# Kernel tuning notes

Hardware: AMD Instinct MI355X
Metric: run time of the kernel (lower is better)

## Reference

```python
import jax, jax.numpy as jnp
import numpy as np

NH = 12   # num_heads
EPS = 1e-6


def _layer_norm(x):
    m = jnp.mean(x, axis=-1, keepdims=True)
    v = jnp.mean((x - m) ** 2, axis=-1, keepdims=True)
    return (x - m) * jax.lax.rsqrt(v + EPS)


def _rms_norm(x, w):
    return x * jax.lax.rsqrt(jnp.mean(x * x, axis=-1, keepdims=True) + EPS) * w


def _rope_cos_sin(f, h, w, head_dim):
    # matches rope_params + calculate_freqs_i: split c=head_dim//2 complex freqs
    # into [c-2*(c//3), c//3, c//3] for the (F,H,W) axes.
    c = head_dim // 2
    inv = 1.0 / (10000.0 ** (np.arange(0, head_dim, 2, dtype=np.float64) / head_dim))
    c1 = c - 2 * (c // 3); c2 = c // 3
    af = np.outer(np.arange(f), inv[:c1])
    ah = np.outer(np.arange(h), inv[c1:c1 + c2])
    aw = np.outer(np.arange(w), inv[c1 + c2:])
    ang = np.concatenate([
        np.broadcast_to(af[:, None, None, :], (f, h, w, c1)),
        np.broadcast_to(ah[None, :, None, :], (f, h, w, c2)),
        np.broadcast_to(aw[None, None, :, :], (f, h, w, c2)),
    ], axis=-1).reshape(f * h * w, c)
    return jnp.asarray(np.cos(ang), jnp.float32), jnp.asarray(np.sin(ang), jnp.float32)


def _apply_rope(x, cos, sin):
    # complex rotation on interleaved pairs; x: [B,L,n,d]
    B, L, n, d = x.shape
    xr = x.reshape(B, L, n, d // 2, 2)
    x0, x1 = xr[..., 0], xr[..., 1]
    co = cos[None, :, None, :]; si = sin[None, :, None, :]
    return jnp.stack([x0 * co - x1 * si, x0 * si + x1 * co], axis=-1).reshape(B, L, n, d)


def _attention(q, k, v):
    scale = 1.0 / jnp.sqrt(jnp.asarray(q.shape[-1], q.dtype))
    s = jnp.einsum('blnd,bmnd->bnlm', q, k) * scale
    return jnp.einsum('bnlm,bmnd->blnd', jax.nn.softmax(s, axis=-1), v)


def _block(x, e, context, mod, sa_wq, sa_bq, sa_wk, sa_bk, sa_wv, sa_bv, sa_wo, sa_bo,
           sa_nq, sa_nk, n3_w, n3_b, ca_wq, ca_bq, ca_wk, ca_bk, ca_wv, ca_bv, ca_wo,
           ca_bo, ca_nq, ca_nk, ffn_w1, ffn_b1, ffn_w2, ffn_b2, f, h, w):
    B, L, C = x.shape
    D = C // NH
    em = mod + e                      # [B,6,C] AdaLN shift/scale/gate params
    cos, sin = _rope_cos_sin(f, h, w, D)
    # --- self-attention with AdaLN modulation + RoPE + qk RMSNorm ---
    xa = _layer_norm(x) * (1.0 + em[:, 1:2]) + em[:, 0:1]
    q = _rms_norm(xa @ sa_wq + sa_bq, sa_nq).reshape(B, L, NH, D)
    k = _rms_norm(xa @ sa_wk + sa_bk, sa_nk).reshape(B, L, NH, D)
    v = (xa @ sa_wv + sa_bv).reshape(B, L, NH, D)
    q = _apply_rope(q, cos, sin)
    k = _apply_rope(k, cos, sin)
    y = _attention(q, k, v).reshape(B, L, C) @ sa_wo + sa_bo
    x = x + y * em[:, 2:3]
    # --- t2v cross-attention (norm3 is affine LayerNorm) ---
    L2 = context.shape[1]
    xc = _layer_norm(x) * n3_w + n3_b
    q = _rms_norm(xc @ ca_wq + ca_bq, ca_nq).reshape(B, L, NH, D)
    k = _rms_norm(context @ ca_wk + ca_bk, ca_nk).reshape(B, L2, NH, D)
    v = (context @ ca_wv + ca_bv).reshape(B, L2, NH, D)
    x = x + (_attention(q, k, v).reshape(B, L, C) @ ca_wo + ca_bo)
    # --- FFN (GELU-tanh) with AdaLN modulation ---
    xf = _layer_norm(x) * (1.0 + em[:, 4:5]) + em[:, 3:4]
    y = jax.nn.gelu(xf @ ffn_w1 + ffn_b1, approximate=True) @ ffn_w2 + ffn_b2
    return x + y * em[:, 5:6]


def setup_inputs() -> dict:
    key = jax.random.key(0)
    ks = jax.random.split(key, 16)
    B, L2, C, FFN = 1, 512, 1536, 8960
    F, H, W = 9, 16, 28
    L = F * H * W  # 4032
    def mk(i, shape, s=0.02):
        return jax.random.normal(ks[i], shape, jnp.float32) * s
    return {
        'x': jax.random.normal(ks[0], (B, L, C), jnp.float32),
        'e': jax.random.normal(ks[1], (B, 6, C), jnp.float32),
        'context': jax.random.normal(ks[2], (B, L2, C), jnp.float32),
        'mod': jax.random.normal(ks[3], (1, 6, C), jnp.float32) / jnp.sqrt(float(C)),
        'sa_wq': mk(4, (C, C)), 'sa_bq': jnp.zeros((C,), jnp.float32),
        'sa_wk': mk(5, (C, C)), 'sa_bk': jnp.zeros((C,), jnp.float32),
        'sa_wv': mk(6, (C, C)), 'sa_bv': jnp.zeros((C,), jnp.float32),
        'sa_wo': mk(7, (C, C)), 'sa_bo': jnp.zeros((C,), jnp.float32),
        'sa_nq': jnp.ones((C,), jnp.float32), 'sa_nk': jnp.ones((C,), jnp.float32),
        'n3_w': jnp.ones((C,), jnp.float32), 'n3_b': jnp.zeros((C,), jnp.float32),
        'ca_wq': mk(8, (C, C)), 'ca_bq': jnp.zeros((C,), jnp.float32),
        'ca_wk': mk(9, (C, C)), 'ca_bk': jnp.zeros((C,), jnp.float32),
        'ca_wv': mk(10, (C, C)), 'ca_bv': jnp.zeros((C,), jnp.float32),
        'ca_wo': mk(11, (C, C)), 'ca_bo': jnp.zeros((C,), jnp.float32),
        'ca_nq': jnp.ones((C,), jnp.float32), 'ca_nk': jnp.ones((C,), jnp.float32),
        'ffn_w1': mk(12, (C, FFN)), 'ffn_b1': jnp.zeros((FFN,), jnp.float32),
        'ffn_w2': mk(13, (FFN, C)), 'ffn_b2': jnp.zeros((C,), jnp.float32),
        'f': F, 'h': H, 'w': W,
    }


def reference(x, e, context, mod, sa_wq, sa_bq, sa_wk, sa_bk, sa_wv, sa_bv, sa_wo,
              sa_bo, sa_nq, sa_nk, n3_w, n3_b, ca_wq, ca_bq, ca_wk, ca_bk, ca_wv,
              ca_bv, ca_wo, ca_bo, ca_nq, ca_nk, ffn_w1, ffn_b1, ffn_w2, ffn_b2,
              f, h, w):
    return _block(x, e, context, mod, sa_wq, sa_bq, sa_wk, sa_bk, sa_wv, sa_bv,
                  sa_wo, sa_bo, sa_nq, sa_nk, n3_w, n3_b, ca_wq, ca_bq, ca_wk,
                  ca_bk, ca_wv, ca_bv, ca_wo, ca_bo, ca_nq, ca_nk, ffn_w1, ffn_b1,
                  ffn_w2, ffn_b2, f, h, w)
```

## Files before the change

### kernel.cpp

```cpp
#include <hip/hip_runtime.h>
#include <math.h>


#define L_SEQ 4032
#define L_PAD 4096
#define C_DIM 1536
#define L_CTX 512
#define FFN_DIM 8960
#define NHEAD 12
#define DHEAD 128

typedef __attribute__((ext_vector_type(8))) short short8;
typedef __attribute__((ext_vector_type(4))) float floatx4;

__device__ inline unsigned short f2bf(float x) {
  unsigned int u = __float_as_uint(x);
  u += 0x7fffu + ((u >> 16) & 1u);
  return (unsigned short)(u >> 16);
}

__device__ inline float2 block_sum2(float2 v) {
  __shared__ float2 red[4];
#pragma unroll
  for (int o = 32; o > 0; o >>= 1) {
    v.x += __shfl_xor(v.x, o, 64);
    v.y += __shfl_xor(v.y, o, 64);
  }
  int wave = threadIdx.x >> 6;
  if ((threadIdx.x & 63) == 0) red[wave] = v;
  __syncthreads();
  float2 t = make_float2(0.f, 0.f);
#pragma unroll
  for (int i = 0; i < 4; ++i) { t.x += red[i].x; t.y += red[i].y; }
  return t;
}

__global__ void add_kernel(float* __restrict__ o, const float* __restrict__ a,
                           const float* __restrict__ b, int n) {
  int i = blockIdx.x * 256 + threadIdx.x;
  if (i < n) o[i] = a[i] + b[i];
}

__global__ void concat3_kernel(float* __restrict__ o, const float* __restrict__ a,
                               const float* __restrict__ b, const float* __restrict__ c) {
  int i = blockIdx.x * 256 + threadIdx.x;
  if (i < C_DIM) {
    o[i] = a[i];
    o[C_DIM + i] = b[i];
    if (c) o[2 * C_DIM + i] = c[i];
  }
}

__global__ void f32_to_bf16_kernel(unsigned short* __restrict__ o,
                                   const float* __restrict__ in, int n) {
  int i = (blockIdx.x * 256 + threadIdx.x) * 4;
  if (i < n) {
    float4 v = *(const float4*)&in[i];
    ushort4 o4 = {f2bf(v.x), f2bf(v.y), f2bf(v.z), f2bf(v.w)};
    *(ushort4*)&o[i] = o4;
  }
}

__global__ __launch_bounds__(256) void transpose_bf16_kernel(
    const float* __restrict__ W, unsigned short* __restrict__ WT, int K, int N) {
  __shared__ float t[32][33];
  int n0 = blockIdx.x * 32, k0 = blockIdx.y * 32;
  int c = threadIdx.x & 31, r0 = threadIdx.x >> 5;
#pragma unroll
  for (int i = 0; i < 4; ++i) {
    int r = r0 + 8 * i;
    t[r][c] = W[(size_t)(k0 + r) * N + n0 + c];
  }
  __syncthreads();
#pragma unroll
  for (int i = 0; i < 4; ++i) {
    int r = r0 + 8 * i;
    WT[(size_t)(n0 + r) * K + k0 + c] = f2bf(t[c][r]);
  }
}

__global__ __launch_bounds__(256) void transpose_v_kernel(
    const float* __restrict__ V, unsigned short* __restrict__ Vt, int stride, int Lk) {
  __shared__ float t[32][33];
  int k0 = blockIdx.x * 32, c0 = blockIdx.y * 32;
  int c = threadIdx.x & 31, r0 = threadIdx.x >> 5;
#pragma unroll
  for (int i = 0; i < 4; ++i) {
    int r = r0 + 8 * i;
    t[r][c] = V[(size_t)(k0 + r) * stride + c0 + c];
  }
  __syncthreads();
#pragma unroll
  for (int i = 0; i < 4; ++i) {
    int r = r0 + 8 * i;
    Vt[(size_t)(c0 + r) * Lk + k0 + c] = f2bf(t[c][r]);
  }
}

__global__ __launch_bounds__(256) void ln_affine_kernel(
    unsigned short* __restrict__ out, const float* __restrict__ in,
    const float* __restrict__ sc, const float* __restrict__ sh, float addOne) {
  int row = blockIdx.x;
  const float* xr = in + (size_t)row * C_DIM;
  float vals[C_DIM / 256];
  float2 p = make_float2(0.f, 0.f);
  int cnt = 0;
  for (int c = threadIdx.x; c < C_DIM; c += 256) {
    float v = xr[c];
    vals[cnt++] = v;
    p.x += v; p.y += v * v;
  }
  float2 t = block_sum2(p);
  float mean = t.x * (1.f / C_DIM);
  float var = t.y * (1.f / C_DIM) - mean * mean;
  float r = rsqrtf(var + 1e-6f);
  cnt = 0;
  for (int c = threadIdx.x; c < C_DIM; c += 256) {
    float xh = (vals[cnt++] - mean) * r;
    out[(size_t)row * C_DIM + c] = f2bf(xh * (addOne + sc[c]) + sh[c]);
  }
}

template <int ROPE>
__global__ __launch_bounds__(256) void rms_post_kernel(
    unsigned short* __restrict__ obf, const float* __restrict__ in,
    const float* __restrict__ w, const float* __restrict__ cosb,
    const float* __restrict__ sinb, int stride, float ps) {
  int row = blockIdx.x;
  const float* xr = in + (size_t)row * stride;
  int c0 = threadIdx.x * 6;
  float v[6];
  *(float2*)&v[0] = *(const float2*)&xr[c0];
  *(float2*)&v[2] = *(const float2*)&xr[c0 + 2];
  *(float2*)&v[4] = *(const float2*)&xr[c0 + 4];
  float s2 = 0.f;
#pragma unroll
  for (int i = 0; i < 6; ++i) s2 += v[i] * v[i];
  float2 t = block_sum2(make_float2(s2, 0.f));
  float r = rsqrtf(t.x * (1.f / C_DIM) + 1e-6f) * ps;
#pragma unroll
  for (int i = 0; i < 6; ++i) v[i] *= r * w[c0 + i];
  if (ROPE) {
#pragma unroll
    for (int i = 0; i < 3; ++i) {
      int c = c0 + 2 * i;
      int j = (c & 127) >> 1;
      float co = cosb[row * 64 + j], si = sinb[row * 64 + j];
      float a = v[2 * i], b = v[2 * i + 1];
      v[2 * i] = a * co - b * si;
      v[2 * i + 1] = a * si + b * co;
    }
  }
  unsigned short* op = obf + (size_t)row * C_DIM + c0;
  ushort2 o01 = {f2bf(v[0]), f2bf(v[1])};
  ushort2 o23 = {f2bf(v[2]), f2bf(v[3])};
  ushort2 o45 = {f2bf(v[4]), f2bf(v[5])};
  *(ushort2*)&op[0] = o01;
  *(ushort2*)&op[2] = o23;
  *(ushort2*)&op[4] = o45;
}

__global__ void rope_tables_kernel(float* __restrict__ cosb, float* __restrict__ sinb) {
  int l = blockIdx.x, j = threadIdx.x;
  int f = l / (16 * 28);
  int rem = l % (16 * 28);
  int hh = rem / 28, ww = rem % 28;
  double inv = pow(10000.0, -(double)(2 * j) / 128.0);
  double pos = (j < 22) ? (double)f : ((j < 43) ? (double)hh : (double)ww);
  double ang = pos * inv;
  cosb[l * 64 + j] = (float)cos(ang);
  sinb[l * 64 + j] = (float)sin(ang);
}

__device__ inline float gelu_tanh(float x) {
  float x3 = x * x * x;
  return 0.5f * x * (1.f + tanhf(0.79788456080286535588f * (x + 0.044715f * x3)));
}

__device__ inline int xcd_remap(int flat, int nwg) {
  int qq = nwg >> 3, rr = nwg & 7;
  int xcd = flat & 7, idx = flat >> 3;
  return (xcd < rr ? xcd * (qq + 1) : rr * (qq + 1) + (xcd - rr) * qq) + idx;
}

template <int EPI>
__global__ __launch_bounds__(256) void mgemm_kernel(
    const unsigned short* __restrict__ A, const unsigned short* __restrict__ BT,
    const float* __restrict__ bias, void* __restrict__ Cout,
    const float* __restrict__ resid, const float* __restrict__ gate,
    int N, int K, int Mlimit) {
  __shared__ short sA[3][4096];
  __shared__ short sB[3][4096];
  const int tid = threadIdx.x;
  const int wv = tid >> 6, lane = tid & 63;
  const int lm = lane & 15, lq = lane >> 4;
  const int wr = wv >> 1, wc = wv & 1;

  const int gx = gridDim.x;
  int flat = xcd_remap(blockIdx.y * gx + blockIdx.x, gx * gridDim.y);
  const int row0 = (flat / gx) * 128, col0 = (flat % gx) * 128;

  floatx4 zero4 = {0.f, 0.f, 0.f, 0.f};
  floatx4 acc[4][4];
#pragma unroll
  for (int i = 0; i < 4; ++i)
#pragma unroll
    for (int j = 0; j < 4; ++j) acc[i][j] = zero4;

  const unsigned short* Abase = A + ((size_t)row0 + lm) * K + lq * 8;
  const unsigned short* Bbase = BT + ((size_t)col0 + lm) * K + lq * 8;

  auto stage = [&](int buf, int k0) {
#pragma unroll
    for (int t = 0; t < 2; ++t) {
      int g = wv * 2 + t;
      __builtin_amdgcn_global_load_lds(
          (const __attribute__((address_space(1))) void*)(Abase + (size_t)(g * 16) * K + k0),
          (__attribute__((address_space(3))) void*)(sA[buf] + g * 512), 16, 0, 0);
      __builtin_amdgcn_global_load_lds(
          (const __attribute__((address_space(1))) void*)(Bbase + (size_t)(g * 16) * K + k0),
          (__attribute__((address_space(3))) void*)(sB[buf] + g * 512), 16, 0, 0);
    }
  };

  stage(0, 0);
  stage(1, 32);
  asm volatile("s_waitcnt vmcnt(4)" ::: "memory");
  __builtin_amdgcn_s_barrier();
  __builtin_amdgcn_sched_barrier(0);

  int cur = 0;
  const int nk = K >> 5;
  for (int t = 0; t < nk; ++t) {
    int b2 = cur + 2; if (b2 >= 3) b2 -= 3;
    const bool more = (t + 2 < nk);
    if (more) stage(b2, (t + 2) << 5);
    const short* sAc = &sA[cur][0];
    const short* sBc = &sB[cur][0];
    short8 af[4], bfv[4];
#pragma unroll
    for (int mt = 0; mt < 4; ++mt)
      af[mt] = *(const short8*)(sAc + (wr * 4 + mt) * 512 + lane * 8);
#pragma unroll
    for (int nt = 0; nt < 4; ++nt)
      bfv[nt] = *(const short8*)(sBc + (wc * 4 + nt) * 512 + lane * 8);
#pragma unroll
    for (int mt = 0; mt < 4; ++mt)
#pragma unroll
      for (int nt = 0; nt < 4; ++nt)
        acc[mt][nt] = __builtin_amdgcn_mfma_f32_16x16x32_bf16(
            af[mt], bfv[nt], acc[mt][nt], 0, 0, 0);
    __builtin_amdgcn_sched_barrier(0);
    if (more) { asm volatile("s_waitcnt vmcnt(4)" ::: "memory"); }
    else      { asm volatile("s_waitcnt vmcnt(0)" ::: "memory"); }
    __builtin_amdgcn_s_barrier();
    __builtin_amdgcn_sched_barrier(0);
    cur = (cur + 1 == 3) ? 0 : cur + 1;
  }

#pragma unroll
  for (int nt = 0; nt < 4; ++nt) {
    int colg = col0 + wc * 64 + nt * 16 + lm;
    float bv = bias[colg];
    float gv = (EPI == 2 && gate) ? gate[colg] : 1.f;
#pragma unroll
    for (int mt = 0; mt < 4; ++mt) {
#pragma unroll
      for (int r = 0; r < 4; ++r) {
        int rowg = row0 + wr * 64 + mt * 16 + lq * 4 + r;
        if (rowg < Mlimit) {
          float v = acc[mt][nt][r] + bv;
          if (EPI == 1) {
            ((unsigned short*)Cout)[(size_t)rowg * N + colg] = f2bf(gelu_tanh(v));
          } else if (EPI == 2) {
            ((float*)Cout)[(size_t)rowg * N + colg] =
                resid[(size_t)rowg * N + colg] + v * gv;
          } else {
            ((float*)Cout)[(size_t)rowg * N + colg] = v;
          }
        }
      }
    }
  }
}

template <int EPI>
__global__ __launch_bounds__(256) void mgemm_k64_kernel(
    const unsigned short* __restrict__ A, const unsigned short* __restrict__ BT,
    const float* __restrict__ bias, void* __restrict__ Cout,
    const float* __restrict__ resid, const float* __restrict__ gate,
    int N, int K, int Mlimit) {
  __shared__ short sA[2][8192];
  __shared__ short sB[2][8192];
  const int tid = threadIdx.x;
  const int wv = tid >> 6, lane = tid & 63;
  const int lm = lane & 15, lq = lane >> 4;
  const int wr = wv >> 1, wc = wv & 1;

  const int gx = gridDim.x;
  int flat = xcd_remap(blockIdx.y * gx + blockIdx.x, gx * gridDim.y);
  const int row0 = (flat / gx) * 128, col0 = (flat % gx) * 128;

  floatx4 zero4 = {0.f, 0.f, 0.f, 0.f};
  floatx4 acc[4][4];
#pragma unroll
  for (int i = 0; i < 4; ++i)
#pragma unroll
    for (int j = 0; j < 4; ++j) acc[i][j] = zero4;

  const unsigned short* Abase = A + ((size_t)row0 + lm) * K + lq * 8;
  const unsigned short* Bbase = BT + ((size_t)col0 + lm) * K + lq * 8;

  auto stage = [&](int buf, int k0) {
#pragma unroll
    for (int kk = 0; kk < 2; ++kk) {
#pragma unroll
      for (int t = 0; t < 2; ++t) {
        int g = wv * 2 + t;
        __builtin_amdgcn_global_load_lds(
            (const __attribute__((address_space(1))) void*)(Abase + (size_t)(g * 16) * K + k0 + kk * 32),
            (__attribute__((address_space(3))) void*)(sA[buf] + kk * 4096 + g * 512), 16, 0, 0);
        __builtin_amdgcn_global_load_lds(
            (const __attribute__((address_space(1))) void*)(Bbase + (size_t)(g * 16) * K + k0 + kk * 32),
            (__attribute__((address_space(3))) void*)(sB[buf] + kk * 4096 + g * 512), 16, 0, 0);
      }
    }
  };

  stage(0, 0);
  asm volatile("s_waitcnt vmcnt(0)" ::: "memory");
  __builtin_amdgcn_s_barrier();
  __builtin_amdgcn_sched_barrier(0);

  int cur = 0;
  const int nk = K >> 6;
  for (int t = 0; t < nk; ++t) {
    if (t + 1 < nk) stage(cur ^ 1, (t + 1) << 6);
#pragma unroll
    for (int kk = 0; kk < 2; ++kk) {
      const short* sAc = &sA[cur][kk * 4096];
      const short* sBc = &sB[cur][kk * 4096];
      short8 af[4], bfv[4];
#pragma unroll
      for (int mt = 0; mt < 4; ++mt)
        af[mt] = *(const short8*)(sAc + (wr * 4 + mt) * 512 + lane * 8);
#pragma unroll
      for (int nt = 0; nt < 4; ++nt)
        bfv[nt] = *(const short8*)(sBc + (wc * 4 + nt) * 512 + lane * 8);
#pragma unroll
      for (int mt = 0; mt < 4; ++mt)
#pragma unroll
        for (int nt = 0; nt < 4; ++nt)
          acc[mt][nt] = __builtin_amdgcn_mfma_f32_16x16x32_bf16(
              af[mt], bfv[nt], acc[mt][nt], 0, 0, 0);
    }
    __builtin_amdgcn_sched_barrier(0);
    asm volatile("s_waitcnt vmcnt(0)" ::: "memory");
    __builtin_amdgcn_s_barrier();
    __builtin_amdgcn_sched_barrier(0);
    cur ^= 1;
  }

#pragma unroll
  for (int nt = 0; nt < 4; ++nt) {
    int colg = col0 + wc * 64 + nt * 16 + lm;
    float bv = bias[colg];
    float gv = (EPI == 2 && gate) ? gate[colg] : 1.f;
#pragma unroll
    for (int mt = 0; mt < 4; ++mt) {
#pragma unroll
      for (int r = 0; r < 4; ++r) {
        int rowg = row0 + wr * 64 + mt * 16 + lq * 4 + r;
        if (rowg < Mlimit) {
          float v = acc[mt][nt][r] + bv;
          if (EPI == 1) {
            ((unsigned short*)Cout)[(size_t)rowg * N + colg] = f2bf(gelu_tanh(v));
          } else if (EPI == 2) {
            ((float*)Cout)[(size_t)rowg * N + colg] =
                resid[(size_t)rowg * N + colg] + v * gv;
          } else {
            ((float*)Cout)[(size_t)rowg * N + colg] = v;
          }
        }
      }
    }
  }
}

template <int EPI>
__global__ __launch_bounds__(256) void mgemm64_kernel(
    const unsigned short* __restrict__ A, const unsigned short* __restrict__ BT,
    const float* __restrict__ bias, void* __restrict__ Cout,
    const float* __restrict__ resid, const float* __restrict__ gate,
    int N, int K, int Mlimit) {
  __shared__ short sA[3][2048];
  __shared__ short sB[3][4096];
  const int tid = threadIdx.x;
  const int wv = tid >> 6, lane = tid & 63;
  const int lm = lane & 15, lq = lane >> 4;
  const int wc = wv;

  const int gx = gridDim.x;
  int flat = xcd_remap(blockIdx.y * gx + blockIdx.x, gx * gridDim.y);
  const int row0 = (flat / gx) * 64, col0 = (flat % gx) * 128;

  floatx4 zero4 = {0.f, 0.f, 0.f, 0.f};
  floatx4 acc[4][2];
#pragma unroll
  for (int i = 0; i < 4; ++i)
#pragma unroll
    for (int j = 0; j < 2; ++j) acc[i][j] = zero4;

  const unsigned short* Abase = A + ((size_t)row0 + lm) * K + lq * 8;
  const unsigned short* Bbase = BT + ((size_t)col0 + lm) * K + lq * 8;

  auto stage = [&](int buf, int k0) {
    __builtin_amdgcn_global_load_lds(
        (const __attribute__((address_space(1))) void*)(Abase + (size_t)(wv * 16) * K + k0),
        (__attribute__((address_space(3))) void*)(sA[buf] + wv * 512), 16, 0, 0);
#pragma unroll
    for (int t = 0; t < 2; ++t) {
      int g = wv * 2 + t;
      __builtin_amdgcn_global_load_lds(
          (const __attribute__((address_space(1))) void*)(Bbase + (size_t)(g * 16) * K + k0),
          (__attribute__((address_space(3))) void*)(sB[buf] + g * 512), 16, 0, 0);
    }
  };

  stage(0, 0);
  stage(1, 32);
  asm volatile("s_waitcnt vmcnt(3)" ::: "memory");
  __builtin_amdgcn_s_barrier();
  __builtin_amdgcn_sched_barrier(0);

  int cur = 0;
  const int nk = K >> 5;
  for (int t = 0; t < nk; ++t) {
    int b2 = cur + 2; if (b2 >= 3) b2 -= 3;
    const bool more = (t + 2 < nk);
    if (more) stage(b2, (t + 2) << 5);
    const short* sAc = &sA[cur][0];
    const short* sBc = &sB[cur][0];
    short8 af[4], bfv[2];
#pragma unroll
    for (int mt = 0; mt < 4; ++mt)
      af[mt] = *(const short8*)(sAc + mt * 512 + lane * 8);
#pragma unroll
    for (int nt = 0; nt < 2; ++nt)
      bfv[nt] = *(const short8*)(sBc + (wc * 2 + nt) * 512 + lane * 8);
#pragma unroll
    for (int mt = 0; mt < 4; ++mt)
#pragma unroll
      for (int nt = 0; nt < 2; ++nt)
        acc[mt][nt] = __builtin_amdgcn_mfma_f32_16x16x32_bf16(
            af[mt], bfv[nt], acc[mt][nt], 0, 0, 0);
    __builtin_amdgcn_sched_barrier(0);
    if (more) { asm volatile("s_waitcnt vmcnt(3)" ::: "memory"); }
    else      { asm volatile("s_waitcnt vmcnt(0)" ::: "memory"); }
    __builtin_amdgcn_s_barrier();
    __builtin_amdgcn_sched_barrier(0);
    cur = (cur + 1 == 3) ? 0 : cur + 1;
  }

#pragma unroll
  for (int nt = 0; nt < 2; ++nt) {
    int colg = col0 + wc * 32 + nt * 16 + lm;
    float bv = bias[colg];
    float gv = (EPI == 2 && gate) ? gate[colg] : 1.f;
#pragma unroll
    for (int mt = 0; mt < 4; ++mt) {
#pragma unroll
      for (int r = 0; r < 4; ++r) {
        int rowg = row0 + mt * 16 + lq * 4 + r;
        if (rowg < Mlimit) {
          float v = acc[mt][nt][r] + bv;
          if (EPI == 1) {
            ((unsigned short*)Cout)[(size_t)rowg * N + colg] = f2bf(gelu_tanh(v));
          } else if (EPI == 2) {
            ((float*)Cout)[(size_t)rowg * N + colg] =
                resid[(size_t)rowg * N + colg] + v * gv;
          } else {
            ((float*)Cout)[(size_t)rowg * N + colg] = v;
          }
        }
      }
    }
  }
}

__global__ __launch_bounds__(256) void attn_mfma_kernel(
    const unsigned short* __restrict__ Qb, const unsigned short* __restrict__ Kb,
    const unsigned short* __restrict__ Vt, unsigned short* __restrict__ O,
    int Lk) {
  __shared__ short sK[3][4096];
  __shared__ short sV[3][4096];
  __shared__ short sP[4][512];
  const int h = blockIdx.y;
  const int q0 = blockIdx.x * 64;
  const int tid = threadIdx.x;
  const int wv = tid >> 6, lane = tid & 63;
  const int lm = lane & 15, lq = lane >> 4;

  short8 qf[4];
  {
    const unsigned short* qrow =
        Qb + (size_t)(q0 + wv * 16 + lm) * C_DIM + h * DHEAD + lq * 8;
#pragma unroll
    for (int dc = 0; dc < 4; ++dc) qf[dc] = *(const short8*)(qrow + dc * 32);
  }

  floatx4 zero4 = {0.f, 0.f, 0.f, 0.f};
  floatx4 acc[8];
#pragma unroll
  for (int g = 0; g < 8; ++g) acc[g] = zero4;
  float m = -1e30f, l = 0.f;

  auto stageKV = [&](int buf, int k0) {
#pragma unroll
    for (int t = 0; t < 2; ++t) {
      int g = wv * 2 + t;
      int nt_ = g >> 2, dc = g & 3;
      const unsigned short* srck =
          Kb + (size_t)(k0 + nt_ * 16 + lm) * C_DIM + h * DHEAD + dc * 32 + lq * 8;
      __builtin_amdgcn_global_load_lds(
          (const __attribute__((address_space(1))) void*)srck,
          (__attribute__((address_space(3))) void*)(sK[buf] + g * 512), 16, 0, 0);
      const unsigned short* srcv =
          Vt + (size_t)(h * DHEAD + g * 16 + lm) * Lk + k0 + lq * 8;
      __builtin_amdgcn_global_load_lds(
          (const __attribute__((address_space(1))) void*)srcv,
          (__attribute__((address_space(3))) void*)(sV[buf] + g * 512), 16, 0, 0);
    }
  };

  stageKV(0, 0);
  stageKV(1, 32);
  asm volatile("s_waitcnt vmcnt(4)" ::: "memory");
  __builtin_amdgcn_s_barrier();
  __builtin_amdgcn_sched_barrier(0);

  int cur = 0;
  const int nsteps = Lk >> 5;
  for (int t = 0; t < nsteps; ++t) {
    int b2 = cur + 2; if (b2 >= 3) b2 -= 3;
    const bool more = (t + 2 < nsteps);
    if (more) stageKV(b2, (t + 2) << 5);
    const short* sKc = &sK[cur][0];
    const short* sVc = &sV[cur][0];

    floatx4 s0 = zero4, s1 = zero4;
#pragma unroll
    for (int dc = 0; dc < 4; ++dc) {
      short8 kf0 = *(const short8*)(sKc + dc * 512 + lane * 8);
      short8 kf1 = *(const short8*)(sKc + (4 + dc) * 512 + lane * 8);
      s0 = __builtin_amdgcn_mfma_f32_16x16x32_bf16(kf0, qf[dc], s0, 0, 0, 0);
      s1 = __builtin_amdgcn_mfma_f32_16x16x32_bf16(kf1, qf[dc], s1, 0, 0, 0);
    }

    float mx = fmaxf(fmaxf(fmaxf(s0[0], s0[1]), fmaxf(s0[2], s0[3])),
                     fmaxf(fmaxf(s1[0], s1[1]), fmaxf(s1[2], s1[3])));
    mx = fmaxf(mx, __shfl_xor(mx, 16));
    mx = fmaxf(mx, __shfl_xor(mx, 32));
    bool need = mx > m + 11.5f;
    if (__any((int)need)) {
      float mn = fmaxf(m, mx);
      float al = exp2f(m - mn);
      m = mn;
      l *= al;
      float ar[4];
#pragma unroll
      for (int r = 0; r < 4; ++r) ar[r] = __shfl(al, lq * 4 + r);
#pragma unroll
      for (int g = 0; g < 8; ++g)
#pragma unroll
        for (int r = 0; r < 4; ++r) acc[g][r] *= ar[r];
    }
    float rs = 0.f;
    ushort4 pk0, pk1;
#pragma unroll
    for (int r = 0; r < 4; ++r) {
      float p = exp2f(s0[r] - m);
      rs += p;
      ((unsigned short*)&pk0)[r] = f2bf(p);
    }
#pragma unroll
    for (int r = 0; r < 4; ++r) {
      float p = exp2f(s1[r] - m);
      rs += p;
      ((unsigned short*)&pk1)[r] = f2bf(p);
    }
    rs += __shfl_xor(rs, 16);
    rs += __shfl_xor(rs, 32);
    l += rs;
    {
      int baseq = (((lq >> 1) * 16 + lm) << 3) + ((lq & 1) << 2);
      *(ushort4*)&sP[wv][baseq] = pk0;
      *(ushort4*)&sP[wv][baseq + 256] = pk1;
    }
    asm volatile("" ::: "memory");
    short8 pa = *(const short8*)(&sP[wv][lane * 8]);
#pragma unroll
    for (int g = 0; g < 8; ++g) {
      short8 vf = *(const short8*)(sVc + g * 512 + lane * 8);
      acc[g] = __builtin_amdgcn_mfma_f32_16x16x32_bf16(pa, vf, acc[g], 0, 0, 0);
    }
    __builtin_amdgcn_sched_barrier(0);
    if (more) { asm volatile("s_waitcnt vmcnt(4)" ::: "memory"); }
    else      { asm volatile("s_waitcnt vmcnt(0)" ::: "memory"); }
    __builtin_amdgcn_s_barrier();
    __builtin_amdgcn_sched_barrier(0);
    cur = (cur + 1 == 3) ? 0 : cur + 1;
  }

  float invl[4];
#pragma unroll
  for (int r = 0; r < 4; ++r) invl[r] = 1.f / __shfl(l, lq * 4 + r);
  unsigned short* orow =
      O + (size_t)(q0 + wv * 16 + lq * 4) * C_DIM + h * DHEAD + lm;
#pragma unroll
  for (int g = 0; g < 8; ++g) {
#pragma unroll
    for (int r = 0; r < 4; ++r) {
      orow[(size_t)r * C_DIM + g * 16] = f2bf(acc[g][r] * invl[r]);
    }
  }
}

extern "C" void kernel_launch(void* const* d_in, const int* in_sizes, int n_in,
                              void* d_out, int out_size, void* d_ws, size_t ws_size,
                              hipStream_t stream) {
  const float* x     = (const float*)d_in[0];
  const float* e     = (const float*)d_in[1];
  const float* ctx   = (const float*)d_in[2];
  const float* mod   = (const float*)d_in[3];
  const float* sa_wq = (const float*)d_in[4];
  const float* sa_bq = (const float*)d_in[5];
  const float* sa_wk = (const float*)d_in[6];
  const float* sa_bk = (const float*)d_in[7];
  const float* sa_wv = (const float*)d_in[8];
  const float* sa_bv = (const float*)d_in[9];
  const float* sa_wo = (const float*)d_in[10];
  const float* sa_bo = (const float*)d_in[11];
  const float* sa_nq = (const float*)d_in[12];
  const float* sa_nk = (const float*)d_in[13];
  const float* n3_w  = (const float*)d_in[14];
  const float* n3_b  = (const float*)d_in[15];
  const float* ca_wq = (const float*)d_in[16];
  const float* ca_bq = (const float*)d_in[17];
  const float* ca_wk = (const float*)d_in[18];
  const float* ca_bk = (const float*)d_in[19];
  const float* ca_wv = (const float*)d_in[20];
  const float* ca_bv = (const float*)d_in[21];
  const float* ca_wo = (const float*)d_in[22];
  const float* ca_bo = (const float*)d_in[23];
  const float* ca_nq = (const float*)d_in[24];
  const float* ca_nk = (const float*)d_in[25];
  const float* ffn_w1 = (const float*)d_in[26];
  const float* ffn_b1 = (const float*)d_in[27];
  const float* ffn_w2 = (const float*)d_in[28];
  const float* ffn_b2 = (const float*)d_in[29];
  float* out = (float*)d_out;

  char* wsb = (char*)d_ws;
  auto alloc_f = [&](size_t n) { float* p = (float*)wsb; wsb += ((n * 4 + 255) / 256) * 256; return p; };
  auto alloc_h = [&](size_t n) { unsigned short* p = (unsigned short*)wsb; wsb += ((n * 2 + 255) / 256) * 256; return p; };

  float* em   = alloc_f(6 * C_DIM);
  float* cosb = alloc_f(L_SEQ * 64);
  float* sinb = alloc_f(L_SEQ * 64);
  float* qkv  = alloc_f((size_t)L_SEQ * 3 * C_DIM);
  float* x1b  = alloc_f((size_t)L_SEQ * C_DIM);
  unsigned short* act_bf  = alloc_h((size_t)L_PAD * C_DIM);
  unsigned short* ctx_bf  = alloc_h((size_t)L_CTX * C_DIM);
  unsigned short* wtqkv = alloc_h((size_t)3 * C_DIM * C_DIM);
  unsigned short* wto   = alloc_h((size_t)C_DIM * C_DIM);
  unsigned short* wtcq  = alloc_h((size_t)C_DIM * C_DIM);
  unsigned short* wtckv = alloc_h((size_t)2 * C_DIM * C_DIM);
  unsigned short* wtco  = alloc_h((size_t)C_DIM * C_DIM);
  unsigned short* wt1   = alloc_h((size_t)FFN_DIM * C_DIM);
  unsigned short* wt2   = alloc_h((size_t)C_DIM * FFN_DIM);
  float* qkv_bias = alloc_f(3 * C_DIM);
  float* ckv_bias = alloc_f(2 * C_DIM);
  unsigned short* kbf_x = alloc_h((size_t)L_CTX * C_DIM);
  unsigned short* vtx   = alloc_h((size_t)C_DIM * L_CTX);

  unsigned short* qbf_self = (unsigned short*)x1b;
  unsigned short* kbf_self = ((unsigned short*)x1b) + (size_t)L_SEQ * C_DIM;
  unsigned short* vt_self  = (unsigned short*)out;
  unsigned short* qbf_x    = (unsigned short*)out;
  float* crossq = qkv;
  float* ckv    = qkv + (size_t)L_SEQ * C_DIM;
  unsigned short* ffnh_bf = (unsigned short*)qkv;

  const float qscale = 0.12751649737103347f;

  dim3 gT(C_DIM / 32, C_DIM / 32);
  dim3 gQKV(3 * C_DIM / 128, L_PAD / 128);
  dim3 gGL64(C_DIM / 128, L_PAD / 64);
  dim3 gCKV64(2 * C_DIM / 128, L_CTX / 64);
  dim3 gAtt(L_SEQ / 64, NHEAD);

  transpose_bf16_kernel<<<gT, 256, 0, stream>>>(sa_wq, wtqkv, C_DIM, C_DIM);
  transpose_bf16_kernel<<<gT, 256, 0, stream>>>(sa_wk, wtqkv + (size_t)C_DIM * C_DIM, C_DIM, C_DIM);
  transpose_bf16_kernel<<<gT, 256, 0, stream>>>(sa_wv, wtqkv + (size_t)2 * C_DIM * C_DIM, C_DIM, C_DIM);
  transpose_bf16_kernel<<<gT, 256, 0, stream>>>(sa_wo, wto, C_DIM, C_DIM);
  transpose_bf16_kernel<<<gT, 256, 0, stream>>>(ca_wq, wtcq, C_DIM, C_DIM);
  transpose_bf16_kernel<<<gT, 256, 0, stream>>>(ca_wk, wtckv, C_DIM, C_DIM);
  transpose_bf16_kernel<<<gT, 256, 0, stream>>>(ca_wv, wtckv + (size_t)C_DIM * C_DIM, C_DIM, C_DIM);
  transpose_bf16_kernel<<<gT, 256, 0, stream>>>(ca_wo, wtco, C_DIM, C_DIM);
  transpose_bf16_kernel<<<dim3(FFN_DIM / 32, C_DIM / 32), 256, 0, stream>>>(ffn_w1, wt1, C_DIM, FFN_DIM);
  transpose_bf16_kernel<<<dim3(C_DIM / 32, FFN_DIM / 32), 256, 0, stream>>>(ffn_w2, wt2, FFN_DIM, C_DIM);
  f32_to_bf16_kernel<<<(L_CTX * C_DIM) / 1024, 256, 0, stream>>>(ctx_bf, ctx, L_CTX * C_DIM);
  concat3_kernel<<<6, 256, 0, stream>>>(qkv_bias, sa_bq, sa_bk, sa_bv);
  concat3_kernel<<<6, 256, 0, stream>>>(ckv_bias, ca_bk, ca_bv, nullptr);

  add_kernel<<<(6 * C_DIM + 255) / 256, 256, 0, stream>>>(em, e, mod, 6 * C_DIM);
  rope_tables_kernel<<<L_SEQ, 64, 0, stream>>>(cosb, sinb);

  ln_affine_kernel<<<L_SEQ, 256, 0, stream>>>(act_bf, x, em + C_DIM, em, 1.f);
  mgemm_kernel<0><<<gQKV, 256, 0, stream>>>(act_bf, wtqkv, qkv_bias, qkv,
                                            nullptr, nullptr, 3 * C_DIM, C_DIM, L_SEQ);
  rms_post_kernel<1><<<L_SEQ, 256, 0, stream>>>(qbf_self, qkv, sa_nq, cosb, sinb,
                                                3 * C_DIM, qscale);
  rms_post_kernel<1><<<L_SEQ, 256, 0, stream>>>(kbf_self, qkv + C_DIM, sa_nk, cosb, sinb,
                                                3 * C_DIM, 1.f);
  transpose_v_kernel<<<dim3(L_SEQ / 32, C_DIM / 32), 256, 0, stream>>>(
      qkv + 2 * C_DIM, vt_self, 3 * C_DIM, L_SEQ);
  attn_mfma_kernel<<<gAtt, 256, 0, stream>>>(qbf_self, kbf_self, vt_self, act_bf, L_SEQ);
  mgemm64_kernel<2><<<gGL64, 256, 0, stream>>>(act_bf, wto, sa_bo, x1b,
                                               x, em + 2 * C_DIM, C_DIM, C_DIM, L_SEQ);

  ln_affine_kernel<<<L_SEQ, 256, 0, stream>>>(act_bf, x1b, n3_w, n3_b, 0.f);
  mgemm64_kernel<0><<<gGL64, 256, 0, stream>>>(act_bf, wtcq, ca_bq, crossq,
                                               nullptr, nullptr, C_DIM, C_DIM, L_SEQ);
  rms_post_kernel<0><<<L_SEQ, 256, 0, stream>>>(qbf_x, crossq, ca_nq, cosb, sinb,
                                                C_DIM, qscale);
  mgemm64_kernel<0><<<gCKV64, 256, 0, stream>>>(ctx_bf, wtckv, ckv_bias, ckv,
                                                nullptr, nullptr, 2 * C_DIM, C_DIM, L_CTX);
  rms_post_kernel<0><<<L_CTX, 256, 0, stream>>>(kbf_x, ckv, ca_nk, cosb, sinb,
                                                2 * C_DIM, 1.f);
  transpose_v_kernel<<<dim3(L_CTX / 32, C_DIM / 32), 256, 0, stream>>>(
      ckv + C_DIM, vtx, 2 * C_DIM, L_CTX);
  attn_mfma_kernel<<<gAtt, 256, 0, stream>>>(qbf_x, kbf_x, vtx, act_bf, L_CTX);
  mgemm64_kernel<2><<<gGL64, 256, 0, stream>>>(act_bf, wtco, ca_bo, out,
                                               x1b, nullptr, C_DIM, C_DIM, L_SEQ);

  ln_affine_kernel<<<L_SEQ, 256, 0, stream>>>(act_bf, out, em + 4 * C_DIM, em + 3 * C_DIM, 1.f);
  dim3 g1(FFN_DIM / 128, L_PAD / 128);
  mgemm_kernel<1><<<g1, 256, 0, stream>>>(act_bf, wt1, ffn_b1, ffnh_bf,
                                          nullptr, nullptr, FFN_DIM, C_DIM, L_SEQ);
  dim3 g2(C_DIM / 128, L_PAD / 128);
  mgemm_k64_kernel<2><<<g2, 256, 0, stream>>>(ffnh_bf, wt2, ffn_b2, out,
                                              out, em + 5 * C_DIM, C_DIM, FFN_DIM, L_SEQ);
}
```

Baseline: 1.530 ms.

## Store QKV projection in bf16 and add banded tile rasterization for GEMMs

```diff
diff --git a/kernel.cpp b/kernel.cpp
--- a/kernel.cpp
+++ b/kernel.cpp
@@ -18,6 +18,9 @@
   u += 0x7fffu + ((u >> 16) & 1u);
   return (unsigned short)(u >> 16);
 }
+__device__ inline float bf2f(unsigned short u) {
+  return __uint_as_float((unsigned int)u << 16);
+}
 
 __device__ inline float2 block_sum2(float2 v) {
   __shared__ float2 red[4];
@@ -94,6 +97,25 @@
   for (int i = 0; i < 4; ++i) {
     int r = r0 + 8 * i;
     Vt[(size_t)(c0 + r) * Lk + k0 + c] = f2bf(t[c][r]);
+  }
+}
+
+__global__ __launch_bounds__(256) void transpose_v_bf_kernel(
+    const unsigned short* __restrict__ V, unsigned short* __restrict__ Vt,
+    int stride, int Lk) {
+  __shared__ unsigned short t[32][33];
+  int k0 = blockIdx.x * 32, c0 = blockIdx.y * 32;
+  int c = threadIdx.x & 31, r0 = threadIdx.x >> 5;
+#pragma unroll
+  for (int i = 0; i < 4; ++i) {
+    int r = r0 + 8 * i;
+    t[r][c] = V[(size_t)(k0 + r) * stride + c0 + c];
+  }
+  __syncthreads();
+#pragma unroll
+  for (int i = 0; i < 4; ++i) {
+    int r = r0 + 8 * i;
+    Vt[(size_t)(c0 + r) * Lk + k0 + c] = t[c][r];
   }
 }
 
@@ -160,6 +182,45 @@
   *(ushort2*)&op[4] = o45;
 }
 
+template <int ROPE>
+__global__ __launch_bounds__(256) void rms_post_bf_kernel(
+    unsigned short* __restrict__ obf, const unsigned short* __restrict__ in,
+    const float* __restrict__ w, const float* __restrict__ cosb,
+    const float* __restrict__ sinb, int stride, float ps) {
+  int row = blockIdx.x;
+  const unsigned short* xr = in + (size_t)row * stride;
+  int c0 = threadIdx.x * 6;
+  ushort2 a0 = *(const ushort2*)&xr[c0];
+  ushort2 a1 = *(const ushort2*)&xr[c0 + 2];
+  ushort2 a2 = *(const ushort2*)&xr[c0 + 4];
+  float v[6] = {bf2f(a0.x), bf2f(a0.y), bf2f(a1.x), bf2f(a1.y), bf2f(a2.x), bf2f(a2.y)};
+  float s2 = 0.f;
+#pragma unroll
+  for (int i = 0; i < 6; ++i) s2 += v[i] * v[i];
+  float2 t = block_sum2(make_float2(s2, 0.f));
+  float r = rsqrtf(t.x * (1.f / C_DIM) + 1e-6f) * ps;
+#pragma unroll
+  for (int i = 0; i < 6; ++i) v[i] *= r * w[c0 + i];
+  if (ROPE) {
+#pragma unroll
+    for (int i = 0; i < 3; ++i) {
+      int c = c0 + 2 * i;
+      int j = (c & 127) >> 1;
+      float co = cosb[row * 64 + j], si = sinb[row * 64 + j];
+      float a = v[2 * i], b = v[2 * i + 1];
+      v[2 * i] = a * co - b * si;
+      v[2 * i + 1] = a * si + b * co;
+    }
+  }
+  unsigned short* op = obf + (size_t)row * C_DIM + c0;
+  ushort2 o01 = {f2bf(v[0]), f2bf(v[1])};
+  ushort2 o23 = {f2bf(v[2]), f2bf(v[3])};
+  ushort2 o45 = {f2bf(v[4]), f2bf(v[5])};
+  *(ushort2*)&op[0] = o01;
+  *(ushort2*)&op[2] = o23;
+  *(ushort2*)&op[4] = o45;
+}
+
 __global__ void rope_tables_kernel(float* __restrict__ cosb, float* __restrict__ sinb) {
   int l = blockIdx.x, j = threadIdx.x;
   int f = l / (16 * 28);
@@ -181,6 +242,21 @@
   int qq = nwg >> 3, rr = nwg & 7;
   int xcd = flat & 7, idx = flat >> 3;
   return (xcd < rr ? xcd * (qq + 1) : rr * (qq + 1) + (xcd - rr) * qq) + idx;
+}
+
+__device__ inline void tile_coords(int gx, int gy, int& tx, int& ty) {
+  int nwg = gx * gy;
+  int flat = xcd_remap(blockIdx.y * gx + blockIdx.x, nwg);
+  if ((gy & 7) == 0) {
+    int bandw = gx << 3;
+    int b = flat / bandw;
+    int r = flat - b * bandw;
+    tx = r >> 3;
+    ty = (b << 3) + (r & 7);
+  } else {
+    ty = flat / gx;
+    tx = flat - ty * gx;
+  }
 }
 
 template <int EPI>
@@ -196,9 +272,9 @@
   const int lm = lane & 15, lq = lane >> 4;
   const int wr = wv >> 1, wc = wv & 1;
 
-  const int gx = gridDim.x;
-  int flat = xcd_remap(blockIdx.y * gx + blockIdx.x, gx * gridDim.y);
-  const int row0 = (flat / gx) * 128, col0 = (flat % gx) * 128;
+  int tx, ty;
+  tile_coords(gridDim.x, gridDim.y, tx, ty);
+  const int row0 = ty * 128, col0 = tx * 128;
 
   floatx4 zero4 = {0.f, 0.f, 0.f, 0.f};
   floatx4 acc[4][4];
@@ -275,6 +351,8 @@
           } else if (EPI == 2) {
             ((float*)Cout)[(size_t)rowg * N + colg] =
                 resid[(size_t)rowg * N + colg] + v * gv;
+          } else if (EPI == 3) {
+            ((unsigned short*)Cout)[(size_t)rowg * N + colg] = f2bf(v);
           } else {
             ((float*)Cout)[(size_t)rowg * N + colg] = v;
           }
@@ -297,9 +375,9 @@
   const int lm = lane & 15, lq = lane >> 4;
   const int wr = wv >> 1, wc = wv & 1;
 
-  const int gx = gridDim.x;
-  int flat = xcd_remap(blockIdx.y * gx + blockIdx.x, gx * gridDim.y);
-  const int row0 = (flat / gx) * 128, col0 = (flat % gx) * 128;
+  int tx, ty;
+  tile_coords(gridDim.x, gridDim.y, tx, ty);
+  const int row0 = ty * 128, col0 = tx * 128;
 
   floatx4 zero4 = {0.f, 0.f, 0.f, 0.f};
   floatx4 acc[4][4];
@@ -378,6 +456,8 @@
           } else if (EPI == 2) {
             ((float*)Cout)[(size_t)rowg * N + colg] =
                 resid[(size_t)rowg * N + colg] + v * gv;
+          } else if (EPI == 3) {
+            ((unsigned short*)Cout)[(size_t)rowg * N + colg] = f2bf(v);
           } else {
             ((float*)Cout)[(size_t)rowg * N + colg] = v;
           }
@@ -400,9 +480,9 @@
   const int lm = lane & 15, lq = lane >> 4;
   const int wc = wv;
 
-  const int gx = gridDim.x;
-  int flat = xcd_remap(blockIdx.y * gx + blockIdx.x, gx * gridDim.y);
-  const int row0 = (flat / gx) * 64, col0 = (flat % gx) * 128;
+  int tx, ty;
+  tile_coords(gridDim.x, gridDim.y, tx, ty);
+  const int row0 = ty * 64, col0 = tx * 128;
 
   floatx4 zero4 = {0.f, 0.f, 0.f, 0.f};
   floatx4 acc[4][2];
@@ -479,6 +559,8 @@
           } else if (EPI == 2) {
             ((float*)Cout)[(size_t)rowg * N + colg] =
                 resid[(size_t)rowg * N + colg] + v * gv;
+          } else if (EPI == 3) {
+            ((unsigned short*)Cout)[(size_t)rowg * N + colg] = f2bf(v);
           } else {
             ((float*)Cout)[(size_t)rowg * N + colg] = v;
           }
@@ -684,6 +766,7 @@
   unsigned short* kbf_x = alloc_h((size_t)L_CTX * C_DIM);
   unsigned short* vtx   = alloc_h((size_t)C_DIM * L_CTX);
 
+  unsigned short* qkvh     = (unsigned short*)qkv;
   unsigned short* qbf_self = (unsigned short*)x1b;
   unsigned short* kbf_self = ((unsigned short*)x1b) + (size_t)L_SEQ * C_DIM;
   unsigned short* vt_self  = (unsigned short*)out;
@@ -718,14 +801,14 @@
   rope_tables_kernel<<<L_SEQ, 64, 0, stream>>>(cosb, sinb);
 
   ln_affine_kernel<<<L_SEQ, 256, 0, stream>>>(act_bf, x, em + C_DIM, em, 1.f);
-  mgemm_kernel<0><<<gQKV, 256, 0, stream>>>(act_bf, wtqkv, qkv_bias, qkv,
+  mgemm_kernel<3><<<gQKV, 256, 0, stream>>>(act_bf, wtqkv, qkv_bias, qkvh,
                                             nullptr, nullptr, 3 * C_DIM, C_DIM, L_SEQ);
-  rms_post_kernel<1><<<L_SEQ, 256, 0, stream>>>(qbf_self, qkv, sa_nq, cosb, sinb,
-                                                3 * C_DIM, qscale);
-  rms_post_kernel<1><<<L_SEQ, 256, 0, stream>>>(kbf_self, qkv + C_DIM, sa_nk, cosb, sinb,
-                                                3 * C_DIM, 1.f);
-  transpose_v_kernel<<<dim3(L_SEQ / 32, C_DIM / 32), 256, 0, stream>>>(
-      qkv + 2 * C_DIM, vt_self, 3 * C_DIM, L_SEQ);
+  rms_post_bf_kernel<1><<<L_SEQ, 256, 0, stream>>>(qbf_self, qkvh, sa_nq, cosb, sinb,
+                                                   3 * C_DIM, qscale);
+  rms_post_bf_kernel<1><<<L_SEQ, 256, 0, stream>>>(kbf_self, qkvh + C_DIM, sa_nk, cosb, sinb,
+                                                   3 * C_DIM, 1.f);
+  transpose_v_bf_kernel<<<dim3(L_SEQ / 32, C_DIM / 32), 256, 0, stream>>>(
+      qkvh + 2 * C_DIM, vt_self, 3 * C_DIM, L_SEQ);
   attn_mfma_kernel<<<gAtt, 256, 0, stream>>>(qbf_self, kbf_self, vt_self, act_bf, L_SEQ);
   mgemm64_kernel<2><<<gGL64, 256, 0, stream>>>(act_bf, wto, sa_bo, x1b,
                                                x, em + 2 * C_DIM, C_DIM, C_DIM, L_SEQ);
```

Result: no change. 1.554 ms (+1.6%).
